# Optimization experiments

Hardware: AMD Instinct MI355X
Metric: run time of the kernel (lower is better)

The kernel has to match this reference:

```python
import jax, jax.numpy as jnp
import numpy as np

D_MODEL = 1024
N_HEAD = 16
ATT_DIM = D_MODEL // N_HEAD


def setup_inputs() -> dict:
    key = jax.random.key(0)
    ks = jax.random.split(key, 7)
    B, S = 2, 2048
    q = jax.random.normal(ks[0], (B, S, D_MODEL), dtype=jnp.float32)
    k = jax.random.normal(ks[1], (B, S, D_MODEL), dtype=jnp.float32)
    v = jax.random.normal(ks[2], (B, S, D_MODEL), dtype=jnp.float32)
    # per-head projection weights, stored as [H, d_model, att_dim] (x @ W form)
    scale_qkv = float(np.sqrt(6.0 / (D_MODEL + ATT_DIM)))  # xavier_uniform
    Wq = jax.random.uniform(ks[3], (N_HEAD, D_MODEL, ATT_DIM), jnp.float32, -scale_qkv, scale_qkv)
    Wk = jax.random.uniform(ks[4], (N_HEAD, D_MODEL, ATT_DIM), jnp.float32, -scale_qkv, scale_qkv)
    Wv = jax.random.uniform(ks[5], (N_HEAD, D_MODEL, ATT_DIM), jnp.float32, -scale_qkv, scale_qkv)
    scale_o = float(np.sqrt(6.0 / (D_MODEL + D_MODEL)))
    Wo = jax.random.uniform(ks[6], (D_MODEL, D_MODEL), jnp.float32, -scale_o, scale_o)
    return {"q": q, "k": k, "v": v, "Wq": Wq, "Wk": Wk, "Wv": Wv, "Wo": Wo}


def reference(q, k, v, Wq, Wk, Wv, Wo):
    # per-head projections, batched over heads: [H,B,S,E]
    qh = jnp.einsum('bsd,hde->hbse', q, Wq)
    kh = jnp.einsum('bsd,hde->hbse', k, Wk)
    vh = jnp.einsum('bsd,hde->hbse', v, Wv)
    # NOTE: original divides by att_dim (not sqrt(att_dim))
    scores = jnp.einsum('hbqe,hbke->hbqk', qh, kh) / ATT_DIM
    attn = jax.nn.softmax(scores, axis=-1)  # [H,B,Sq,Sk]
    att = jnp.einsum('hbqk,hbke->hbqe', attn, vh)  # [H,B,S,E]
    # concat heads along last dim in head order, then output projection
    H, B, S, E = att.shape
    cat = jnp.transpose(att, (1, 2, 0, 3)).reshape(B, S, H * E)
    out = cat @ Wo  # dropout is identity in eval
    return (out, attn)
```

## Files before the change

kernel.cpp:

```cpp
#include <hip/hip_runtime.h>
#include <hip/hip_bf16.h>

#define DM 1024
#define NH 16
#define AD 64
#define BB 2
#define SS 2048
#define LOG2E 1.44269504f

typedef float f32x4 __attribute__((ext_vector_type(4)));
typedef short bf16x8 __attribute__((ext_vector_type(8)));
typedef unsigned short u16;
typedef unsigned int u32;
typedef u16 u16x4 __attribute__((ext_vector_type(4)));
typedef u16 u16x8 __attribute__((ext_vector_type(8)));
typedef u32 u32x4 __attribute__((ext_vector_type(4)));

static __device__ __forceinline__ u16 f2bf(float f) {
  unsigned u = __builtin_bit_cast(unsigned, f);
  u += 0x7fffu + ((u >> 16) & 1u);
  return (u16)(u >> 16);
}

#define MFMA16(a, b, c) __builtin_amdgcn_mfma_f32_16x16x32_bf16((a), (b), (c), 0, 0, 0)

static __device__ __forceinline__ void ld_lds16(const void* g, void* l) {
  __builtin_amdgcn_global_load_lds((const __attribute__((address_space(1))) u32*)g,
                                   (__attribute__((address_space(3))) u32*)l, 16, 0, 0);
}

#define WAITV(N)                                             \
  do {                                                       \
    asm volatile("s_waitcnt vmcnt(" #N ")" ::: "memory");    \
    __builtin_amdgcn_sched_barrier(0);                       \
  } while (0)
#define WAITL0()                                             \
  do {                                                       \
    asm volatile("s_waitcnt lgkmcnt(0)" ::: "memory");       \
    __builtin_amdgcn_sched_barrier(0);                       \
  } while (0)
#define BAR() __builtin_amdgcn_s_barrier()

#define KFRAG(buf, row, P) (*(const bf16x8*)(&(buf)[(row) * 64 + ((((P) ^ ((row) & 7))) << 3)]))
#define V64(buf, row, P, hh) \
  (*(const u16x4*)(&(buf)[(row) * 64 + ((((P) ^ ((row) & 7))) << 3) + (hh) * 4]))

__global__ __launch_bounds__(256, 4) void cast3_kernel(const float* __restrict__ s0,
                                                       const float* __restrict__ s1,
                                                       const float* __restrict__ s2,
                                                       u16* __restrict__ d0, u16* __restrict__ d1,
                                                       u16* __restrict__ d2, int n8) {
  const float* src = blockIdx.y == 0 ? s0 : blockIdx.y == 1 ? s1 : s2;
  u16* dst = blockIdx.y == 0 ? d0 : blockIdx.y == 1 ? d1 : d2;
  int i = blockIdx.x * blockDim.x + threadIdx.x;
  int stride = gridDim.x * blockDim.x;
  for (; i < n8; i += stride) {
    const f32x4* p = (const f32x4*)src + 2 * (size_t)i;
    f32x4 a = p[0], b = p[1];
    u16x8 o;
    o[0] = f2bf(a[0]); o[1] = f2bf(a[1]); o[2] = f2bf(a[2]); o[3] = f2bf(a[3]);
    o[4] = f2bf(b[0]); o[5] = f2bf(b[1]); o[6] = f2bf(b[2]); o[7] = f2bf(b[3]);
    *((u16x8*)dst + i) = o;
  }
}

template <int MODE>
__global__ __launch_bounds__(256, 4) void tcast_kernel(const float* __restrict__ s0,
                                                       const float* __restrict__ s1,
                                                       const float* __restrict__ s2,
                                                       u16* __restrict__ dst, int R, int C,
                                                       float scale0) {
  __shared__ float T[64][65];
  const float* src;
  u16* dstp;
  float scale;
  long bo;
  if (MODE == 0) {
    src = s0; bo = (long)blockIdx.z * R * C; dstp = dst; scale = scale0;
  } else {
    int which = blockIdx.z >> 4, zz = blockIdx.z & 15;
    src = which == 0 ? s0 : which == 1 ? s1 : s2;
    bo = (long)zz * R * C;
    dstp = dst + (long)which * NH * R * C;
    scale = which == 0 ? scale0 : 1.0f;
  }
  int r0 = blockIdx.x * 64, c0 = blockIdx.y * 64;
  int cl = threadIdx.x & 63, rl = threadIdx.x >> 6;
#pragma unroll
  for (int i = 0; i < 16; i++) {
    int rr = rl + 4 * i;
    T[cl][rr] = src[bo + (long)(r0 + rr) * C + c0 + cl];
  }
  __syncthreads();
#pragma unroll
  for (int i = 0; i < 16; i++) {
    int cc = rl + 4 * i;
    dstp[bo + (long)(c0 + cc) * R + r0 + cl] = f2bf(T[cc][cl] * scale);
  }
}

template <int MODE>
__global__ __launch_bounds__(256, 2) void proj_kernel(const u16* __restrict__ X,
                                                      const u16* __restrict__ WT,
                                                      void* __restrict__ outp, long ob, long oh,
                                                      long os, long oe) {
  __shared__ u16 Ab[2][128 * 64];
  __shared__ u16 Bb[2][128 * 64];
  int s0 = blockIdx.x * 128, n0 = blockIdx.y * 128, b = blockIdx.z;
  int tid = threadIdx.x, w = tid >> 6, lane = tid & 63, g = lane >> 4, li = lane & 15;
  int wr = (w >> 1) * 64, wc = (w & 1) * 64;
  const u16* xb = X + ((long)b * SS + s0) * DM;
  const u16* wb = WT + (long)n0 * DM;
  const u16* asrc[4];
  const u16* bsrc[4];
  u16* adst[2][4];
  u16* bdst[2][4];
#pragma unroll
  for (int i = 0; i < 4; i++) {
    int cc = i * 256 + tid;
    int row = cc >> 3, sp = (cc ^ (row & 7)) & 7;
    asrc[i] = xb + (long)row * DM + sp * 8;
    bsrc[i] = wb + (long)row * DM + sp * 8;
    adst[0][i] = &Ab[0][cc * 8]; adst[1][i] = &Ab[1][cc * 8];
    bdst[0][i] = &Bb[0][cc * 8]; bdst[1][i] = &Bb[1][cc * 8];
  }

#pragma unroll
  for (int i = 0; i < 4; i++) ld_lds16(asrc[i], adst[0][i]);
#pragma unroll
  for (int i = 0; i < 4; i++) ld_lds16(bsrc[i], bdst[0][i]);

  f32x4 acc[4][4] = {};
  for (int kc = 0; kc < DM / 64; kc++) {
    int cur = kc & 1;
    if (kc + 1 < DM / 64) {
      int ko = (kc + 1) * 64;
#pragma unroll
      for (int i = 0; i < 4; i++) ld_lds16(asrc[i] + ko, adst[cur ^ 1][i]);
#pragma unroll
      for (int i = 0; i < 4; i++) ld_lds16(bsrc[i] + ko, bdst[cur ^ 1][i]);
      WAITV(8);
    } else {
      WAITV(0);
    }
    BAR();
    const u16* ab = Ab[cur];
    const u16* bb = Bb[cur];
#pragma unroll
    for (int kk = 0; kk < 2; kk++) {
      bf16x8 bf[4];
#pragma unroll
      for (int j = 0; j < 4; j++) bf[j] = KFRAG(bb, wc + j * 16 + li, kk * 4 + g);
#pragma unroll
      for (int mi = 0; mi < 4; mi++) {
        bf16x8 af = KFRAG(ab, wr + mi * 16 + li, kk * 4 + g);
#pragma unroll
        for (int j = 0; j < 4; j++) acc[mi][j] = MFMA16(af, bf[j], acc[mi][j]);
      }
    }
    WAITL0();
    BAR();
  }

  long bh = (long)b * ob;
#pragma unroll
  for (int mi = 0; mi < 4; mi++) {
    int sb = s0 + wr + mi * 16 + 4 * g;
#pragma unroll
    for (int j = 0; j < 4; j++) {
      int col = n0 + wc + j * 16 + li;
      if (MODE == 0) {
        u16* o = (u16*)outp;
        long idx = bh + (long)(col >> 6) * oh + (long)(col & 63) * oe;
#pragma unroll
        for (int r = 0; r < 4; r++) o[idx + (long)(sb + r) * os] = f2bf(acc[mi][j][r]);
      } else if (MODE == 1) {
        u16x4 vv;
#pragma unroll
        for (int r = 0; r < 4; r++) vv[r] = f2bf(acc[mi][j][r]);
        *(u16x4*)((u16*)outp + bh + (long)(col >> 6) * oh + (long)(col & 63) * oe + sb) = vv;
      } else {
        float* o = (float*)outp;
#pragma unroll
        for (int r = 0; r < 4; r++) o[bh + (long)(sb + r) * os + col] = acc[mi][j][r];
      }
    }
  }
}

__global__ __launch_bounds__(512, 4) void attn_kernel(const u16* __restrict__ qh,
                                                      const u16* __restrict__ kh,
                                                      const u16* __restrict__ vhT,
                                                      float* __restrict__ attn_out,
                                                      u16* __restrict__ cat) {
  __shared__ u16 Kb[2][64 * 64];
  __shared__ u16 Vb[2][64 * 64];
  int h = blockIdx.y, b = blockIdx.z;
  int hb = h * BB + b;
  int tid = threadIdx.x;
  int w = tid >> 6, lane = tid & 63;
  int g = lane >> 4, li = lane & 15;
  long base = (long)hb * SS * AD;
  const u16* qhb = qh + base;
  const u16* khb = kh + base;
  const u16* vhb = vhT + base;
  int q0 = blockIdx.x * 128 + w * 16;

  bf16x8 bq0 = *(const bf16x8*)(qhb + (q0 + li) * AD + 8 * g);
  bf16x8 bq1 = *(const bf16x8*)(qhb + (q0 + li) * AD + 32 + 8 * g);

  int srow = tid >> 3, spiece = (tid ^ (srow & 7)) & 7;
  const u16* ksrc = khb + (long)srow * AD + spiece * 8;
  const u16* vsrc = vhb + (long)srow * SS + spiece * 8;
  u16* kd0 = &Kb[0][tid * 8]; u16* kd1 = &Kb[1][tid * 8];
  u16* vd0 = &Vb[0][tid * 8]; u16* vd1 = &Vb[1][tid * 8];

  float l_run = 0.f;
  ld_lds16(ksrc, kd0);
  ld_lds16(ksrc + 64 * AD, kd1);
  ld_lds16(ksrc + 2 * 64 * AD, vd0);
  for (int ch4 = 0; ch4 < SS / 64; ch4 += 4) {
#pragma unroll
    for (int u = 0; u < 4; u++) {
      int ch = ch4 + u;
      u16* pdst = ((u + 3) & 3) == 0 ? kd0 : ((u + 3) & 3) == 1 ? kd1
                 : ((u + 3) & 3) == 2 ? vd0 : vd1;
      if (ch + 3 < SS / 64) {
        ld_lds16(ksrc + (ch + 3) * 64 * AD, pdst);
        WAITV(3);
      } else if (ch == SS / 64 - 3) {
        WAITV(2);
      } else if (ch == SS / 64 - 2) {
        WAITV(1);
      } else {
        WAITV(0);
      }
      BAR();
      const u16* kb = u == 0 ? Kb[0] : u == 1 ? Kb[1] : u == 2 ? Vb[0] : Vb[1];
      f32x4 sacc[4] = {};
#pragma unroll
      for (int mi = 0; mi < 4; mi++) {
        bf16x8 a0 = KFRAG(kb, mi * 16 + li, g);
        bf16x8 a1 = KFRAG(kb, mi * 16 + li, 4 + g);
        sacc[mi] = MFMA16(a0, bq0, sacc[mi]);
        sacc[mi] = MFMA16(a1, bq1, sacc[mi]);
      }
#pragma unroll
      for (int c = 0; c < 4; c++)
#pragma unroll
        for (int r = 0; r < 4; r++) l_run += exp2f(sacc[c][r]);
      WAITL0();
      BAR();
    }
  }
  l_run += __shfl_xor(l_run, 16);
  l_run += __shfl_xor(l_run, 32);
  float moff = log2f(l_run);

  ld_lds16(ksrc, kd0);
  ld_lds16(vsrc, vd0);
  f32x4 accv[4] = {};
  float* arow = attn_out + ((long)hb * SS + q0 + li) * SS;
  for (int ch2 = 0; ch2 < SS / 64; ch2 += 2) {
#pragma unroll
    for (int u = 0; u < 2; u++) {
      int ch = ch2 + u;
      u16* kpd = u ? kd0 : kd1;
      u16* vpd = u ? vd0 : vd1;
      if (ch + 1 < SS / 64) {
        ld_lds16(ksrc + (ch + 1) * 64 * AD, kpd);
        ld_lds16(vsrc + (ch + 1) * 64, vpd);
        if (ch == 0) {
          WAITV(2);
        } else {
          WAITV(6);
        }
      } else {
        WAITV(4);
      }
      BAR();
      const u16* kb = Kb[u];
      const u16* vb = Vb[u];
      f32x4 sacc[4] = {};
#pragma unroll
      for (int mi = 0; mi < 4; mi++) {
        bf16x8 a0 = KFRAG(kb, mi * 16 + li, g);
        bf16x8 a1 = KFRAG(kb, mi * 16 + li, 4 + g);
        sacc[mi] = MFMA16(a0, bq0, sacc[mi]);
        sacc[mi] = MFMA16(a1, bq1, sacc[mi]);
      }
      u32 pw[8];
#pragma unroll
      for (int c = 0; c < 4; c++) {
        f32x4 pv;
#pragma unroll
        for (int r = 0; r < 4; r++) pv[r] = exp2f(sacc[c][r] - moff);
        *(f32x4*)(arow + ch * 64 + c * 16 + 4 * g) = pv;
        pw[2 * c] = (u32)f2bf(pv[0]) | ((u32)f2bf(pv[1]) << 16);
        pw[2 * c + 1] = (u32)f2bf(pv[2]) | ((u32)f2bf(pv[3]) << 16);
      }
#pragma unroll
      for (int kk = 0; kk < 2; kk++) {
        u32x4 aw = {pw[4 * kk], pw[4 * kk + 1], pw[4 * kk + 2], pw[4 * kk + 3]};
        bf16x8 ap = __builtin_bit_cast(bf16x8, aw);
#pragma unroll
        for (int et = 0; et < 4; et++) {
          int row = et * 16 + li;
          u16x4 b0 = V64(vb, row, 4 * kk + (g >> 1), g & 1);
          u16x4 b1 = V64(vb, row, 4 * kk + 2 + (g >> 1), g & 1);
          u16x8 ub = {b0[0], b0[1], b0[2], b0[3], b1[0], b1[1], b1[2], b1[3]};
          bf16x8 bv = __builtin_bit_cast(bf16x8, ub);
          accv[et] = MFMA16(ap, bv, accv[et]);
        }
      }
      WAITL0();
      BAR();
    }
  }

#pragma unroll
  for (int et = 0; et < 4; et++)
#pragma unroll
    for (int r = 0; r < 4; r++)
      cat[((long)b * SS + q0 + 4 * g + r) * DM + h * AD + et * 16 + li] = f2bf(accv[et][r]);
}

extern "C" void kernel_launch(void* const* d_in, const int* in_sizes, int n_in, void* d_out,
                              int out_size, void* d_ws, size_t ws_size, hipStream_t stream) {
  const float* q = (const float*)d_in[0];
  const float* k = (const float*)d_in[1];
  const float* v = (const float*)d_in[2];
  const float* Wq = (const float*)d_in[3];
  const float* Wk = (const float*)d_in[4];
  const float* Wv = (const float*)d_in[5];
  const float* Wo = (const float*)d_in[6];
  float* out = (float*)d_out;
  float* attn_out = out + (long)BB * SS * DM;

  const long NX = (long)BB * SS * DM;
  const long NW = (long)NH * DM * AD;
  u16* ws = (u16*)d_ws;
  u16* xq = ws;
  u16* xk = xq + NX;
  u16* xv = xk + NX;
  u16* WqT = xv + NX;
  u16* WkT = WqT + NW;
  u16* WvT = WkT + NW;
  u16* WoT = WvT + NW;
  u16* qhw = WoT + (long)DM * DM;
  u16* khw = qhw + NX;
  u16* vhw = khw + NX;
  u16* catw = vhw + NX;

  cast3_kernel<<<dim3(700, 3), 256, 0, stream>>>(q, k, v, xq, xk, xv, (int)(NX / 8));
  tcast_kernel<1><<<dim3(16, 1, 48), 256, 0, stream>>>(Wq, Wk, Wv, WqT, DM, AD, LOG2E / AD);
  tcast_kernel<0><<<dim3(16, 16, 1), 256, 0, stream>>>(Wo, nullptr, nullptr, WoT, DM, DM, 1.0f);

  dim3 pg(SS / 128, DM / 128, BB);
  proj_kernel<0><<<pg, 256, 0, stream>>>(xq, WqT, qhw, (long)SS * AD, (long)BB * SS * AD, AD, 1);
  proj_kernel<0><<<pg, 256, 0, stream>>>(xk, WkT, khw, (long)SS * AD, (long)BB * SS * AD, AD, 1);
  proj_kernel<1><<<pg, 256, 0, stream>>>(xv, WvT, vhw, (long)SS * AD, (long)BB * SS * AD, 1, SS);

  attn_kernel<<<dim3(SS / 128, NH, BB), 512, 0, stream>>>(qhw, khw, vhw, attn_out, catw);

  proj_kernel<2><<<pg, 256, 0, stream>>>(catw, WoT, out, (long)SS * DM, 0, DM, 0);
}
```

Before: 294.3 us.

## Fuse Q/K/V projections into one launch and use 128x64 GEMM tiles

Measured after the change: 283.6 us. -3.6%, faster.

```diff
diff --git a/kernel.cpp b/kernel.cpp
--- a/kernel.cpp
+++ b/kernel.cpp
@@ -99,38 +99,49 @@
   }
 }
 
-template <int MODE>
-__global__ __launch_bounds__(256, 2) void proj_kernel(const u16* __restrict__ X,
-                                                      const u16* __restrict__ WT,
-                                                      void* __restrict__ outp, long ob, long oh,
-                                                      long os, long oe) {
+__global__ __launch_bounds__(256, 3) void qkvproj_kernel(const u16* __restrict__ X0,
+                                                         const u16* __restrict__ WT0,
+                                                         u16* __restrict__ out0) {
   __shared__ u16 Ab[2][128 * 64];
-  __shared__ u16 Bb[2][128 * 64];
-  int s0 = blockIdx.x * 128, n0 = blockIdx.y * 128, b = blockIdx.z;
+  __shared__ u16 Bb[2][64 * 64];
+  const long NX = (long)BB * SS * DM;
+  const long NW = (long)NH * DM * AD;
+  int which = blockIdx.z;
+  int sg0 = blockIdx.x * 128;
+  int b = sg0 >> 11, s0 = sg0 & (SS - 1);
+  int h = blockIdx.y;
   int tid = threadIdx.x, w = tid >> 6, lane = tid & 63, g = lane >> 4, li = lane & 15;
-  int wr = (w >> 1) * 64, wc = (w & 1) * 64;
-  const u16* xb = X + ((long)b * SS + s0) * DM;
-  const u16* wb = WT + (long)n0 * DM;
+  const u16* xb = X0 + (long)which * NX + ((long)b * SS + s0) * DM;
+  const u16* wb = WT0 + (long)which * NW + (long)h * 64 * DM;
+  u16* outp = out0 + (long)which * NX;
+
   const u16* asrc[4];
-  const u16* bsrc[4];
   u16* adst[2][4];
-  u16* bdst[2][4];
 #pragma unroll
   for (int i = 0; i < 4; i++) {
     int cc = i * 256 + tid;
     int row = cc >> 3, sp = (cc ^ (row & 7)) & 7;
     asrc[i] = xb + (long)row * DM + sp * 8;
+    adst[0][i] = &Ab[0][cc * 8];
+    adst[1][i] = &Ab[1][cc * 8];
+  }
+  const u16* bsrc[2];
+  u16* bdst[2][2];
+#pragma unroll
+  for (int i = 0; i < 2; i++) {
+    int cc = i * 256 + tid;
+    int row = cc >> 3, sp = (cc ^ (row & 7)) & 7;
     bsrc[i] = wb + (long)row * DM + sp * 8;
-    adst[0][i] = &Ab[0][cc * 8]; adst[1][i] = &Ab[1][cc * 8];
-    bdst[0][i] = &Bb[0][cc * 8]; bdst[1][i] = &Bb[1][cc * 8];
+    bdst[0][i] = &Bb[0][cc * 8];
+    bdst[1][i] = &Bb[1][cc * 8];
   }
 
 #pragma unroll
   for (int i = 0; i < 4; i++) ld_lds16(asrc[i], adst[0][i]);
 #pragma unroll
-  for (int i = 0; i < 4; i++) ld_lds16(bsrc[i], bdst[0][i]);
-
-  f32x4 acc[4][4] = {};
+  for (int i = 0; i < 2; i++) ld_lds16(bsrc[i], bdst[0][i]);
+
+  f32x4 acc[2][4] = {};
   for (int kc = 0; kc < DM / 64; kc++) {
     int cur = kc & 1;
     if (kc + 1 < DM / 64) {
@@ -138,8 +149,8 @@
 #pragma unroll
       for (int i = 0; i < 4; i++) ld_lds16(asrc[i] + ko, adst[cur ^ 1][i]);
 #pragma unroll
-      for (int i = 0; i < 4; i++) ld_lds16(bsrc[i] + ko, bdst[cur ^ 1][i]);
-      WAITV(8);
+      for (int i = 0; i < 2; i++) ld_lds16(bsrc[i] + ko, bdst[cur ^ 1][i]);
+      WAITV(6);
     } else {
       WAITV(0);
     }
@@ -150,10 +161,10 @@
     for (int kk = 0; kk < 2; kk++) {
       bf16x8 bf[4];
 #pragma unroll
-      for (int j = 0; j < 4; j++) bf[j] = KFRAG(bb, wc + j * 16 + li, kk * 4 + g);
-#pragma unroll
-      for (int mi = 0; mi < 4; mi++) {
-        bf16x8 af = KFRAG(ab, wr + mi * 16 + li, kk * 4 + g);
+      for (int j = 0; j < 4; j++) bf[j] = KFRAG(bb, j * 16 + li, kk * 4 + g);
+#pragma unroll
+      for (int mi = 0; mi < 2; mi++) {
+        bf16x8 af = KFRAG(ab, w * 32 + mi * 16 + li, kk * 4 + g);
 #pragma unroll
         for (int j = 0; j < 4; j++) acc[mi][j] = MFMA16(af, bf[j], acc[mi][j]);
       }
@@ -162,28 +173,104 @@
     BAR();
   }
 
-  long bh = (long)b * ob;
-#pragma unroll
-  for (int mi = 0; mi < 4; mi++) {
-    int sb = s0 + wr + mi * 16 + 4 * g;
+  long obase = (long)h * (BB * SS * AD) + (long)b * (SS * AD);
+#pragma unroll
+  for (int mi = 0; mi < 2; mi++) {
+    int sb = s0 + w * 32 + mi * 16 + 4 * g;
 #pragma unroll
     for (int j = 0; j < 4; j++) {
-      int col = n0 + wc + j * 16 + li;
-      if (MODE == 0) {
-        u16* o = (u16*)outp;
-        long idx = bh + (long)(col >> 6) * oh + (long)(col & 63) * oe;
-#pragma unroll
-        for (int r = 0; r < 4; r++) o[idx + (long)(sb + r) * os] = f2bf(acc[mi][j][r]);
-      } else if (MODE == 1) {
+      int e = j * 16 + li;
+      if (which < 2) {
+#pragma unroll
+        for (int r = 0; r < 4; r++)
+          outp[obase + (long)(sb + r) * AD + e] = f2bf(acc[mi][j][r]);
+      } else {
         u16x4 vv;
 #pragma unroll
         for (int r = 0; r < 4; r++) vv[r] = f2bf(acc[mi][j][r]);
-        *(u16x4*)((u16*)outp + bh + (long)(col >> 6) * oh + (long)(col & 63) * oe + sb) = vv;
-      } else {
-        float* o = (float*)outp;
-#pragma unroll
-        for (int r = 0; r < 4; r++) o[bh + (long)(sb + r) * os + col] = acc[mi][j][r];
-      }
+        *(u16x4*)(outp + obase + (long)e * SS + sb) = vv;
+      }
+    }
+  }
+}
+
+__global__ __launch_bounds__(256, 3) void outproj_kernel(const u16* __restrict__ X,
+                                                         const u16* __restrict__ WT,
+                                                         float* __restrict__ out) {
+  __shared__ u16 Ab[2][128 * 64];
+  __shared__ u16 Bb[2][64 * 64];
+  int sg0 = blockIdx.x * 128;
+  int n0 = blockIdx.y * 64;
+  int tid = threadIdx.x, w = tid >> 6, lane = tid & 63, g = lane >> 4, li = lane & 15;
+  const u16* xb = X + (long)sg0 * DM;
+  const u16* wb = WT + (long)n0 * DM;
+
+  const u16* asrc[4];
+  u16* adst[2][4];
+#pragma unroll
+  for (int i = 0; i < 4; i++) {
+    int cc = i * 256 + tid;
+    int row = cc >> 3, sp = (cc ^ (row & 7)) & 7;
+    asrc[i] = xb + (long)row * DM + sp * 8;
+    adst[0][i] = &Ab[0][cc * 8];
+    adst[1][i] = &Ab[1][cc * 8];
+  }
+  const u16* bsrc[2];
+  u16* bdst[2][2];
+#pragma unroll
+  for (int i = 0; i < 2; i++) {
+    int cc = i * 256 + tid;
+    int row = cc >> 3, sp = (cc ^ (row & 7)) & 7;
+    bsrc[i] = wb + (long)row * DM + sp * 8;
+    bdst[0][i] = &Bb[0][cc * 8];
+    bdst[1][i] = &Bb[1][cc * 8];
+  }
+
+#pragma unroll
+  for (int i = 0; i < 4; i++) ld_lds16(asrc[i], adst[0][i]);
+#pragma unroll
+  for (int i = 0; i < 2; i++) ld_lds16(bsrc[i], bdst[0][i]);
+
+  f32x4 acc[2][4] = {};
+  for (int kc = 0; kc < DM / 64; kc++) {
+    int cur = kc & 1;
+    if (kc + 1 < DM / 64) {
+      int ko = (kc + 1) * 64;
+#pragma unroll
+      for (int i = 0; i < 4; i++) ld_lds16(asrc[i] + ko, adst[cur ^ 1][i]);
+#pragma unroll
+      for (int i = 0; i < 2; i++) ld_lds16(bsrc[i] + ko, bdst[cur ^ 1][i]);
+      WAITV(6);
+    } else {
+      WAITV(0);
+    }
+    BAR();
+    const u16* ab = Ab[cur];
+    const u16* bb = Bb[cur];
+#pragma unroll
+    for (int kk = 0; kk < 2; kk++) {
+      bf16x8 bf[4];
+#pragma unroll
+      for (int j = 0; j < 4; j++) bf[j] = KFRAG(bb, j * 16 + li, kk * 4 + g);
+#pragma unroll
+      for (int mi = 0; mi < 2; mi++) {
+        bf16x8 af = KFRAG(ab, w * 32 + mi * 16 + li, kk * 4 + g);
+#pragma unroll
+        for (int j = 0; j < 4; j++) acc[mi][j] = MFMA16(af, bf[j], acc[mi][j]);
+      }
+    }
+    WAITL0();
+    BAR();
+  }
+
+#pragma unroll
+  for (int mi = 0; mi < 2; mi++) {
+    int sb = sg0 + w * 32 + mi * 16 + 4 * g;
+#pragma unroll
+    for (int j = 0; j < 4; j++) {
+      int col = n0 + j * 16 + li;
+#pragma unroll
+      for (int r = 0; r < 4; r++) out[(long)(sb + r) * DM + col] = acc[mi][j][r];
     }
   }
 }
@@ -352,16 +439,15 @@
   u16* vhw = khw + NX;
   u16* catw = vhw + NX;
 
+  (void)xk; (void)xv; (void)WkT; (void)WvT; (void)khw;
+
   cast3_kernel<<<dim3(700, 3), 256, 0, stream>>>(q, k, v, xq, xk, xv, (int)(NX / 8));
   tcast_kernel<1><<<dim3(16, 1, 48), 256, 0, stream>>>(Wq, Wk, Wv, WqT, DM, AD, LOG2E / AD);
   tcast_kernel<0><<<dim3(16, 16, 1), 256, 0, stream>>>(Wo, nullptr, nullptr, WoT, DM, DM, 1.0f);
 
-  dim3 pg(SS / 128, DM / 128, BB);
-  proj_kernel<0><<<pg, 256, 0, stream>>>(xq, WqT, qhw, (long)SS * AD, (long)BB * SS * AD, AD, 1);
-  proj_kernel<0><<<pg, 256, 0, stream>>>(xk, WkT, khw, (long)SS * AD, (long)BB * SS * AD, AD, 1);
-  proj_kernel<1><<<pg, 256, 0, stream>>>(xv, WvT, vhw, (long)SS * AD, (long)BB * SS * AD, 1, SS);
+  qkvproj_kernel<<<dim3(BB * SS / 128, NH, 3), 256, 0, stream>>>(xq, WqT, qhw);
 
   attn_kernel<<<dim3(SS / 128, NH, BB), 512, 0, stream>>>(qhw, khw, vhw, attn_out, catw);
 
-  proj_kernel<2><<<pg, 256, 0, stream>>>(catw, WoT, out, (long)SS * DM, 0, DM, 0);
-}
+  outproj_kernel<<<dim3(BB * SS / 128, DM / 64), 256, 0, stream>>>(catw, WoT, out);
+}
```
